# Optimization experiments

Measured on AMD Instinct MI355X. Metric: run time of the kernel, lower is better.

## Reference

```python
import jax, jax.numpy as jnp
import numpy as np


def setup_inputs() -> dict:
    key = jax.random.key(0)
    ks = jax.random.split(key, 7)
    B, d_model, Hs, Ws = 16, 384, 64, 64
    state_dim, d_inner = 64, 768
    L = Hs * Ws
    return {
        "x": jax.random.normal(ks[0], (B, d_model, L), jnp.float32),
        "w_bcdt": jax.random.normal(ks[1], (3 * state_dim, d_model), jnp.float32) * 0.05,
        "w_dw": jax.random.normal(ks[2], (3 * state_dim, 1, 3, 3), jnp.float32) * 0.3,
        "w_hz": jax.random.normal(ks[3], (2 * d_inner, d_model), jnp.float32) * 0.05,
        "w_out": jax.random.normal(ks[4], (d_model, d_inner), jnp.float32) * 0.05,
        "a_param": jax.random.uniform(ks[5], (state_dim,), jnp.float32, 1.0, 16.0),
        "d_param": jnp.ones((1,), jnp.float32),
        "H": Hs,
        "W": Ws,
    }


def reference(x, w_bcdt, w_dw, w_hz, w_out, a_param, d_param, H, W):
    batch, d_model, L = x.shape
    state_dim = a_param.shape[0]
    d_inner = w_out.shape[1]
    conv_dim = 3 * state_dim

    # 1x1 conv projection: (B, 3*state_dim, L)
    bc_dt = jnp.einsum("od,bdl->bol", w_bcdt, x)
    # depthwise 3x3 conv on the (H, W) spatial grid
    bc_dt = bc_dt.reshape(batch, conv_dim, H, W)
    bc_dt = jax.lax.conv_general_dilated(
        bc_dt, w_dw, window_strides=(1, 1), padding=((1, 1), (1, 1)),
        dimension_numbers=("NCHW", "OIHW", "NCHW"),
        feature_group_count=conv_dim,
    ).reshape(batch, conv_dim, L)

    Bm, Cm, dt = jnp.split(bc_dt, 3, axis=1)  # each (B, state_dim, L)
    A = jax.nn.softmax(dt + a_param[None, :, None], axis=-1)
    AB = A * Bm  # (B, state_dim, L)

    # state aggregation: (B, d_model, state_dim)
    h = jnp.einsum("bdl,bsl->bds", x, AB)
    hz = jnp.einsum("od,bds->bos", w_hz, h)  # (B, 2*d_inner, state_dim)
    h_i, z = jnp.split(hz, 2, axis=1)
    h = jnp.einsum("od,bds->bos", w_out, h_i * jax.nn.silu(z) + h_i * d_param)

    # broadcast state back to tokens: (B, d_model, L)
    y = jnp.einsum("bds,bsl->bdl", h, Cm).reshape(batch, d_model, H, W)
    return y, h
```

## Files before the change

kernel.cpp:

```cpp
#include <hip/hip_runtime.h>
#include <hip/hip_bf16.h>

#define BATCH 16
#define DMODEL 384
#define LTOK 4096
#define SDIM 64
#define C3 192
#define DINNER 768

typedef __attribute__((ext_vector_type(8))) short short8;
typedef __attribute__((ext_vector_type(4))) float f32x4;

__device__ __forceinline__ short f2bf(float f) {
    unsigned u = __builtin_bit_cast(unsigned, f);
    u += 0x7fffu + ((u >> 16) & 1u);
    return (short)(u >> 16);
}

template<int BN, int NF, bool AF32, bool BF32, bool ATOMIC>
__global__ __launch_bounds__(256) void gemm_bf16(
    const void* __restrict__ Ap, const void* __restrict__ Bp, float* __restrict__ Cp,
    int M, int N, int K, long sA, long sB, long sC, int nTilesN, int splitK)
{
    const int b = blockIdx.z;
    const int ntile  = blockIdx.x % nTilesN;
    const int kchunk = blockIdx.x / nTilesN;
    const int row0 = blockIdx.y << 6;
    const int col0 = ntile * BN;
    const int kPer = K / splitK;
    const int kBeg = kchunk * kPer, kEnd = kBeg + kPer;

    __shared__ short As[64][40];
    __shared__ short Bs[BN][40];

    const int t = threadIdx.x;
    const int wid = t >> 6, lane = t & 63;
    const int lr = lane & 15;
    const int lk = (lane >> 4) << 3;

    f32x4 acc[4][NF];
#pragma unroll
    for (int i = 0; i < 4; i++)
#pragma unroll
        for (int j = 0; j < NF; j++)
#pragma unroll
            for (int r = 0; r < 4; r++) acc[i][j][r] = 0.f;

    for (int kt = kBeg; kt < kEnd; kt += 32) {
        {
            const int arow = t >> 2, akb = (t & 3) << 3;
            if constexpr (AF32) {
                const float* s = (const float*)Ap + b * sA + (long)(row0 + arow) * K + kt + akb;
                short8 v;
#pragma unroll
                for (int j = 0; j < 8; j++) v[j] = f2bf(s[j]);
                *(short8*)&As[arow][akb] = v;
            } else {
                const short* s = (const short*)Ap + b * sA + (long)(row0 + arow) * K + kt + akb;
                *(short8*)&As[arow][akb] = *(const short8*)s;
            }
        }
#pragma unroll
        for (int rr = 0; rr < BN / 64; rr++) {
            const int u = t + rr * 256;
            const int brow = u >> 2, bkb = (u & 3) << 3;
            if constexpr (BF32) {
                const float* s = (const float*)Bp + b * sB + (long)(col0 + brow) * K + kt + bkb;
                short8 v;
#pragma unroll
                for (int j = 0; j < 8; j++) v[j] = f2bf(s[j]);
                *(short8*)&Bs[brow][bkb] = v;
            } else {
                const short* s = (const short*)Bp + b * sB + (long)(col0 + brow) * K + kt + bkb;
                *(short8*)&Bs[brow][bkb] = *(const short8*)s;
            }
        }
        __syncthreads();

        short8 af[4], bfr[NF];
#pragma unroll
        for (int mi = 0; mi < 4; mi++) af[mi] = *(const short8*)&As[mi * 16 + lr][lk];
#pragma unroll
        for (int ni = 0; ni < NF; ni++) bfr[ni] = *(const short8*)&Bs[wid * (BN / 4) + ni * 16 + lr][lk];
#pragma unroll
        for (int mi = 0; mi < 4; mi++)
#pragma unroll
            for (int ni = 0; ni < NF; ni++)
                acc[mi][ni] = __builtin_amdgcn_mfma_f32_16x16x32_bf16(af[mi], bfr[ni], acc[mi][ni], 0, 0, 0);
        __syncthreads();
    }

    float* Cb = Cp + b * sC;
#pragma unroll
    for (int mi = 0; mi < 4; mi++)
#pragma unroll
        for (int ni = 0; ni < NF; ni++)
#pragma unroll
            for (int r = 0; r < 4; r++) {
                const long row = row0 + mi * 16 + ((lane >> 4) << 2) + r;
                const long col = col0 + wid * (BN / 4) + ni * 16 + lr;
                if constexpr (ATOMIC) atomicAdd(&Cb[row * N + col], acc[mi][ni][r]);
                else                  Cb[row * N + col] = acc[mi][ni][r];
            }
}

__global__ __launch_bounds__(256) void transpose_x(const float* __restrict__ x, short* __restrict__ xbT)
{
    const int b = blockIdx.z;
    const int l0 = blockIdx.x << 6, d0 = blockIdx.y << 6;
    __shared__ float tl[64][65];
    const int t = threadIdx.x, c = t & 63, r0 = t >> 6;
    const float* ip = x + ((long)b * DMODEL + d0) * LTOK + l0;
    for (int d = r0; d < 64; d += 4) tl[d][c] = ip[(long)d * LTOK + c];
    __syncthreads();
    short* op = xbT + ((long)b * LTOK + l0) * DMODEL + d0;
    for (int l = r0; l < 64; l += 4) op[(long)l * DMODEL + c] = f2bf(tl[c][l]);
}

__global__ __launch_bounds__(256) void dwconv3x3(
    const float* __restrict__ in, const float* __restrict__ w, float* __restrict__ out)
{
    const int bc = blockIdx.x;
    const int c = bc % C3;
    __shared__ float tile[64 * 64];
    __shared__ float wc[9];
    const float* ip = in + (long)bc * 4096;
    for (int i = threadIdx.x; i < 4096; i += 256) tile[i] = ip[i];
    if (threadIdx.x < 9) wc[threadIdx.x] = w[c * 9 + threadIdx.x];
    __syncthreads();
    float* op = out + (long)bc * 4096;
    for (int i = threadIdx.x; i < 4096; i += 256) {
        int y = i >> 6, x = i & 63;
        float s = 0.f;
#pragma unroll
        for (int dy = -1; dy <= 1; dy++)
#pragma unroll
            for (int dx = -1; dx <= 1; dx++) {
                int yy = y + dy, xx = x + dx;
                if (yy >= 0 && yy < 64 && xx >= 0 && xx < 64)
                    s += tile[yy * 64 + xx] * wc[(dy + 1) * 3 + (dx + 1)];
            }
        op[i] = s;
    }
}

__global__ __launch_bounds__(256) void softmax_ab(
    const float* __restrict__ conv, short* __restrict__ AB)
{
    const int b = blockIdx.x >> 6, s = blockIdx.x & 63;
    const float* dt = conv + ((long)b * C3 + 128 + s) * (long)LTOK;
    const float* Bm = conv + ((long)b * C3 + s) * (long)LTOK;
    short* ab = AB + ((long)b * SDIM + s) * (long)LTOK;
    const int t = threadIdx.x;

    float v[16];
    float mx = -1e30f;
#pragma unroll
    for (int i = 0; i < 16; i++) { v[i] = dt[t + i * 256]; mx = fmaxf(mx, v[i]); }
#pragma unroll
    for (int o = 32; o > 0; o >>= 1) mx = fmaxf(mx, __shfl_xor(mx, o));
    __shared__ float redm[4];
    const int wid = t >> 6;
    if ((t & 63) == 0) redm[wid] = mx;
    __syncthreads();
    mx = fmaxf(fmaxf(redm[0], redm[1]), fmaxf(redm[2], redm[3]));

    float sum = 0.f;
#pragma unroll
    for (int i = 0; i < 16; i++) { v[i] = __expf(v[i] - mx); sum += v[i]; }
#pragma unroll
    for (int o = 32; o > 0; o >>= 1) sum += __shfl_xor(sum, o);
    __shared__ float reds[4];
    if ((t & 63) == 0) reds[wid] = sum;
    __syncthreads();
    sum = reds[0] + reds[1] + reds[2] + reds[3];
    const float inv = 1.0f / sum;
#pragma unroll
    for (int i = 0; i < 16; i++)
        ab[t + i * 256] = f2bf(v[i] * inv * Bm[t + i * 256]);
}

__global__ __launch_bounds__(256) void gate_k(
    const float* __restrict__ hzT, const float* __restrict__ d_param, float* __restrict__ gT)
{
    const long i = (long)blockIdx.x * 256 + threadIdx.x;
    const long b = i / (SDIM * DINNER), r = i % (SDIM * DINNER);
    const long s = r / DINNER, o = r % DINNER;
    const float* hp = hzT + b * (SDIM * 2L * DINNER) + s * (2L * DINNER);
    const float hi = hp[o];
    const float z  = hp[DINNER + o];
    const float sil = z / (1.f + __expf(-z));
    gT[i] = hi * (sil + d_param[0]);
}

__global__ __launch_bounds__(256) void transpose_hout(
    const float* __restrict__ houtT, float* __restrict__ hout, short* __restrict__ hb)
{
    const int b = blockIdx.y, d0 = blockIdx.x << 6;
    __shared__ float tl[64][65];
    const int t = threadIdx.x, c = t & 63, r0 = t >> 6;
    const float* ip = houtT + (long)b * SDIM * DMODEL + d0;
    for (int s = r0; s < 64; s += 4) tl[s][c] = ip[(long)s * DMODEL + c];
    __syncthreads();
    float* op = hout + ((long)b * DMODEL + d0) * SDIM;
    short* ob = hb + ((long)b * DMODEL + d0) * SDIM;
    for (int d = r0; d < 64; d += 4) {
        float v = tl[c][d];
        op[(long)d * SDIM + c] = v;
        ob[(long)d * SDIM + c] = f2bf(v);
    }
}

__global__ __launch_bounds__(256) void transpose_cm(
    const float* __restrict__ conv, short* __restrict__ CmT)
{
    const int b = blockIdx.y, l0 = blockIdx.x << 6;
    __shared__ float tl[64][65];
    const int t = threadIdx.x, c = t & 63, r0 = t >> 6;
    const float* ip = conv + ((long)b * C3 + SDIM) * LTOK + l0;
    for (int s = r0; s < 64; s += 4) tl[s][c] = ip[(long)s * LTOK + c];
    __syncthreads();
    short* op = CmT + ((long)b * LTOK + l0) * SDIM;
    for (int l = r0; l < 64; l += 4) op[(long)l * SDIM + c] = f2bf(tl[c][l]);
}

extern "C" void kernel_launch(void* const* d_in, const int* in_sizes, int n_in,
                              void* d_out, int out_size, void* d_ws, size_t ws_size,
                              hipStream_t stream) {
    const float* x      = (const float*)d_in[0];
    const float* w_bcdt = (const float*)d_in[1];
    const float* w_dw   = (const float*)d_in[2];
    const float* w_hz   = (const float*)d_in[3];
    const float* w_out  = (const float*)d_in[4];
    const float* dparam = (const float*)d_in[6];

    char* ws = (char*)d_ws;
    short* xbT  = (short*)ws;
    float* conv = (float*)ws;
    float* bcdt  = (float*)(ws + 50331648);
    short* AB    = (short*)(ws + 50331648);
    short* CmT   = (short*)(ws + 58720256);
    float* hT    = (float*)(ws + 67108864);
    float* hzT   = (float*)(ws + 68681728);
    float* gT    = (float*)(ws + 74973184);
    float* houtT = (float*)(ws + 78118912);
    short* hb    = (short*)(ws + 79691776);

    float* y    = (float*)d_out;
    float* hout = (float*)d_out + 25165824;

    transpose_x<<<dim3(64, 6, 16), 256, 0, stream>>>(x, xbT);

    gemm_bf16<128, 2, true, false, false><<<dim3(32, 3, BATCH), 256, 0, stream>>>(
        w_bcdt, xbT, bcdt, C3, LTOK, DMODEL,
        0L, (long)LTOK * DMODEL, (long)C3 * LTOK, 32, 1);

    dwconv3x3<<<dim3(BATCH * C3), 256, 0, stream>>>(bcdt, w_dw, conv);

    softmax_ab<<<dim3(BATCH * SDIM), 256, 0, stream>>>(conv, AB);

    hipMemsetAsync(hT, 0, (size_t)BATCH * SDIM * DMODEL * 4, stream);
    gemm_bf16<128, 2, false, true, true><<<dim3(3 * 8, 1, BATCH), 256, 0, stream>>>(
        AB, x, hT, SDIM, DMODEL, LTOK,
        (long)SDIM * LTOK, (long)DMODEL * LTOK, (long)SDIM * DMODEL, 3, 8);

    gemm_bf16<128, 2, true, true, false><<<dim3(12, 1, BATCH), 256, 0, stream>>>(
        hT, w_hz, hzT, SDIM, 2 * DINNER, DMODEL,
        (long)SDIM * DMODEL, 0L, (long)SDIM * 2 * DINNER, 12, 1);

    gate_k<<<dim3((BATCH * SDIM * DINNER) / 256), 256, 0, stream>>>(hzT, dparam, gT);

    gemm_bf16<128, 2, true, true, false><<<dim3(3, 1, BATCH), 256, 0, stream>>>(
        gT, w_out, houtT, SDIM, DMODEL, DINNER,
        (long)SDIM * DINNER, 0L, (long)SDIM * DMODEL, 3, 1);

    transpose_hout<<<dim3(6, 16), 256, 0, stream>>>(houtT, hout, hb);

    transpose_cm<<<dim3(64, 16), 256, 0, stream>>>(conv, CmT);

    gemm_bf16<128, 2, false, false, false><<<dim3(32, 6, BATCH), 256, 0, stream>>>(
        hb, CmT, y, DMODEL, LTOK, SDIM,
        (long)DMODEL * SDIM, (long)LTOK * SDIM, (long)DMODEL * LTOK, 32, 1);
}
```

Baseline: 356.3 us.

## Store projection in bf16, fuse depthwise conv into softmax, widen GEMM tiles

The projection GEMM now writes its output as bf16 instead of fp32. The depthwise conv for the B and dt channels is fused into the softmax kernel, which reads the bf16 projection into shared memory and computes both convolutions on the fly, so the fp32 conv intermediate is no longer written and read back. A separate kernel convolves only the Cm channels. The first and last GEMMs use 256-wide N tiles with four fragments per wave. This cuts intermediate memory traffic but adds bf16 rounding before the conv and raises per-block register and LDS use.

```diff
diff --git a/kernel.cpp b/kernel.cpp
--- a/kernel.cpp
+++ b/kernel.cpp
@@ -16,10 +16,13 @@
     u += 0x7fffu + ((u >> 16) & 1u);
     return (short)(u >> 16);
 }
-
-template<int BN, int NF, bool AF32, bool BF32, bool ATOMIC>
+__device__ __forceinline__ float bf2f(short s) {
+    return __builtin_bit_cast(float, ((unsigned)(unsigned short)s) << 16);
+}
+
+template<int BN, int NF, bool AF32, bool BF32, int CMODE>
 __global__ __launch_bounds__(256) void gemm_bf16(
-    const void* __restrict__ Ap, const void* __restrict__ Bp, float* __restrict__ Cp,
+    const void* __restrict__ Ap, const void* __restrict__ Bp, void* __restrict__ Cp,
     int M, int N, int K, long sA, long sB, long sC, int nTilesN, int splitK)
 {
     const int b = blockIdx.z;
@@ -90,7 +93,6 @@
         __syncthreads();
     }
 
-    float* Cb = Cp + b * sC;
 #pragma unroll
     for (int mi = 0; mi < 4; mi++)
 #pragma unroll
@@ -99,8 +101,9 @@
             for (int r = 0; r < 4; r++) {
                 const long row = row0 + mi * 16 + ((lane >> 4) << 2) + r;
                 const long col = col0 + wid * (BN / 4) + ni * 16 + lr;
-                if constexpr (ATOMIC) atomicAdd(&Cb[row * N + col], acc[mi][ni][r]);
-                else                  Cb[row * N + col] = acc[mi][ni][r];
+                if constexpr (CMODE == 1)      atomicAdd((float*)Cp + b * sC + row * N + col, acc[mi][ni][r]);
+                else if constexpr (CMODE == 2) *((short*)Cp + b * sC + row * N + col) = f2bf(acc[mi][ni][r]);
+                else                           *((float*)Cp + b * sC + row * N + col) = acc[mi][ni][r];
             }
 }
 
@@ -117,49 +120,47 @@
     for (int l = r0; l < 64; l += 4) op[(long)l * DMODEL + c] = f2bf(tl[c][l]);
 }
 
-__global__ __launch_bounds__(256) void dwconv3x3(
-    const float* __restrict__ in, const float* __restrict__ w, float* __restrict__ out)
-{
-    const int bc = blockIdx.x;
-    const int c = bc % C3;
-    __shared__ float tile[64 * 64];
-    __shared__ float wc[9];
-    const float* ip = in + (long)bc * 4096;
-    for (int i = threadIdx.x; i < 4096; i += 256) tile[i] = ip[i];
-    if (threadIdx.x < 9) wc[threadIdx.x] = w[c * 9 + threadIdx.x];
-    __syncthreads();
-    float* op = out + (long)bc * 4096;
-    for (int i = threadIdx.x; i < 4096; i += 256) {
-        int y = i >> 6, x = i & 63;
-        float s = 0.f;
+__global__ __launch_bounds__(256) void conv_softmax_ab(
+    const short* __restrict__ bcdt, const float* __restrict__ w_dw, short* __restrict__ AB)
+{
+    const int b = blockIdx.x >> 6, s = blockIdx.x & 63;
+    __shared__ float pB[4096];
+    __shared__ float pD[4096];
+    __shared__ float wB[9], wD[9];
+    __shared__ float redm[4], reds[4];
+    const int t = threadIdx.x;
+
+    const short* srcB = bcdt + ((long)b * C3 + s) * 4096;
+    const short* srcD = bcdt + ((long)b * C3 + 128 + s) * 4096;
+#pragma unroll
+    for (int j = 0; j < 2; j++) {
+        const int o = (t + j * 256) * 8;
+        short8 vb = *(const short8*)(srcB + o);
+        short8 vd = *(const short8*)(srcD + o);
+#pragma unroll
+        for (int e = 0; e < 8; e++) { pB[o + e] = bf2f(vb[e]); pD[o + e] = bf2f(vd[e]); }
+    }
+    if (t < 9) { wB[t] = w_dw[s * 9 + t]; wD[t] = w_dw[(128 + s) * 9 + t]; }
+    __syncthreads();
+
+    float v[16];
+    float mx = -1e30f;
+#pragma unroll
+    for (int i = 0; i < 16; i++) {
+        const int l = t + i * 256, y = l >> 6, x = l & 63;
+        float sacc = 0.f;
 #pragma unroll
         for (int dy = -1; dy <= 1; dy++)
 #pragma unroll
             for (int dx = -1; dx <= 1; dx++) {
                 int yy = y + dy, xx = x + dx;
                 if (yy >= 0 && yy < 64 && xx >= 0 && xx < 64)
-                    s += tile[yy * 64 + xx] * wc[(dy + 1) * 3 + (dx + 1)];
-            }
-        op[i] = s;
-    }
-}
-
-__global__ __launch_bounds__(256) void softmax_ab(
-    const float* __restrict__ conv, short* __restrict__ AB)
-{
-    const int b = blockIdx.x >> 6, s = blockIdx.x & 63;
-    const float* dt = conv + ((long)b * C3 + 128 + s) * (long)LTOK;
-    const float* Bm = conv + ((long)b * C3 + s) * (long)LTOK;
-    short* ab = AB + ((long)b * SDIM + s) * (long)LTOK;
-    const int t = threadIdx.x;
-
-    float v[16];
-    float mx = -1e30f;
-#pragma unroll
-    for (int i = 0; i < 16; i++) { v[i] = dt[t + i * 256]; mx = fmaxf(mx, v[i]); }
+                    sacc += pD[yy * 64 + xx] * wD[(dy + 1) * 3 + (dx + 1)];
+            }
+        v[i] = sacc; mx = fmaxf(mx, sacc);
+    }
 #pragma unroll
     for (int o = 32; o > 0; o >>= 1) mx = fmaxf(mx, __shfl_xor(mx, o));
-    __shared__ float redm[4];
     const int wid = t >> 6;
     if ((t & 63) == 0) redm[wid] = mx;
     __syncthreads();
@@ -170,14 +171,73 @@
     for (int i = 0; i < 16; i++) { v[i] = __expf(v[i] - mx); sum += v[i]; }
 #pragma unroll
     for (int o = 32; o > 0; o >>= 1) sum += __shfl_xor(sum, o);
-    __shared__ float reds[4];
     if ((t & 63) == 0) reds[wid] = sum;
     __syncthreads();
     sum = reds[0] + reds[1] + reds[2] + reds[3];
     const float inv = 1.0f / sum;
-#pragma unroll
-    for (int i = 0; i < 16; i++)
-        ab[t + i * 256] = f2bf(v[i] * inv * Bm[t + i * 256]);
+
+    short* ab = AB + ((long)b * SDIM + s) * (long)LTOK;
+#pragma unroll
+    for (int i = 0; i < 16; i++) {
+        const int l = t + i * 256, y = l >> 6, x = l & 63;
+        float uacc = 0.f;
+#pragma unroll
+        for (int dy = -1; dy <= 1; dy++)
+#pragma unroll
+            for (int dx = -1; dx <= 1; dx++) {
+                int yy = y + dy, xx = x + dx;
+                if (yy >= 0 && yy < 64 && xx >= 0 && xx < 64)
+                    uacc += pB[yy * 64 + xx] * wB[(dy + 1) * 3 + (dx + 1)];
+            }
+        ab[l] = f2bf(v[i] * inv * uacc);
+    }
+}
+
+__global__ __launch_bounds__(256) void dwconv_cm(
+    const short* __restrict__ bcdt, const float* __restrict__ w, float* __restrict__ convCm)
+{
+    const int bc = blockIdx.x;
+    const int b = bc >> 6, cc = bc & 63;
+    __shared__ float tile[4096];
+    __shared__ float wc[9];
+    const short* ip = bcdt + ((long)b * C3 + 64 + cc) * 4096;
+    const int t = threadIdx.x;
+#pragma unroll
+    for (int j = 0; j < 2; j++) {
+        const int o = (t + j * 256) * 8;
+        short8 vv = *(const short8*)(ip + o);
+#pragma unroll
+        for (int e = 0; e < 8; e++) tile[o + e] = bf2f(vv[e]);
+    }
+    if (t < 9) wc[t] = w[(64 + cc) * 9 + t];
+    __syncthreads();
+    float* op = convCm + (long)bc * 4096;
+    for (int i = t; i < 4096; i += 256) {
+        int y = i >> 6, x = i & 63;
+        float sacc = 0.f;
+#pragma unroll
+        for (int dy = -1; dy <= 1; dy++)
+#pragma unroll
+            for (int dx = -1; dx <= 1; dx++) {
+                int yy = y + dy, xx = x + dx;
+                if (yy >= 0 && yy < 64 && xx >= 0 && xx < 64)
+                    sacc += tile[yy * 64 + xx] * wc[(dy + 1) * 3 + (dx + 1)];
+            }
+        op[i] = sacc;
+    }
+}
+
+__global__ __launch_bounds__(256) void transpose_cm(
+    const float* __restrict__ convCm, short* __restrict__ CmT)
+{
+    const int b = blockIdx.y, l0 = blockIdx.x << 6;
+    __shared__ float tl[64][65];
+    const int t = threadIdx.x, c = t & 63, r0 = t >> 6;
+    const float* ip = convCm + (long)b * SDIM * LTOK + l0;
+    for (int s = r0; s < 64; s += 4) tl[s][c] = ip[(long)s * LTOK + c];
+    __syncthreads();
+    short* op = CmT + ((long)b * LTOK + l0) * SDIM;
+    for (int l = r0; l < 64; l += 4) op[(long)l * SDIM + c] = f2bf(tl[c][l]);
 }
 
 __global__ __launch_bounds__(256) void gate_k(
@@ -209,19 +269,6 @@
         op[(long)d * SDIM + c] = v;
         ob[(long)d * SDIM + c] = f2bf(v);
     }
-}
-
-__global__ __launch_bounds__(256) void transpose_cm(
-    const float* __restrict__ conv, short* __restrict__ CmT)
-{
-    const int b = blockIdx.y, l0 = blockIdx.x << 6;
-    __shared__ float tl[64][65];
-    const int t = threadIdx.x, c = t & 63, r0 = t >> 6;
-    const float* ip = conv + ((long)b * C3 + SDIM) * LTOK + l0;
-    for (int s = r0; s < 64; s += 4) tl[s][c] = ip[(long)s * LTOK + c];
-    __syncthreads();
-    short* op = CmT + ((long)b * LTOK + l0) * SDIM;
-    for (int l = r0; l < 64; l += 4) op[(long)l * SDIM + c] = f2bf(tl[c][l]);
 }
 
 extern "C" void kernel_launch(void* const* d_in, const int* in_sizes, int n_in,
@@ -235,50 +282,50 @@
     const float* dparam = (const float*)d_in[6];
 
     char* ws = (char*)d_ws;
-    short* xbT  = (short*)ws;
-    float* conv = (float*)ws;
-    float* bcdt  = (float*)(ws + 50331648);
-    short* AB    = (short*)(ws + 50331648);
-    short* CmT   = (short*)(ws + 58720256);
-    float* hT    = (float*)(ws + 67108864);
-    float* hzT   = (float*)(ws + 68681728);
-    float* gT    = (float*)(ws + 74973184);
-    float* houtT = (float*)(ws + 78118912);
-    short* hb    = (short*)(ws + 79691776);
+    short* xbT    = (short*)(ws);
+    short* bcdt   = (short*)(ws + 50331648);
+    short* AB     = (short*)(ws + 75497472);
+    float* convCm = (float*)(ws + 83886080);
+    short* CmT    = (short*)(ws + 100663296);
+    float* hT     = (float*)(ws + 109051904);
+    float* hzT    = (float*)(ws + 110624768);
+    float* gT     = (float*)(ws + 116916224);
+    float* houtT  = (float*)(ws + 120061952);
+    short* hb     = (short*)(ws + 121634816);
 
     float* y    = (float*)d_out;
     float* hout = (float*)d_out + 25165824;
 
     transpose_x<<<dim3(64, 6, 16), 256, 0, stream>>>(x, xbT);
 
-    gemm_bf16<128, 2, true, false, false><<<dim3(32, 3, BATCH), 256, 0, stream>>>(
+    gemm_bf16<256, 4, true, false, 2><<<dim3(16, 3, BATCH), 256, 0, stream>>>(
         w_bcdt, xbT, bcdt, C3, LTOK, DMODEL,
-        0L, (long)LTOK * DMODEL, (long)C3 * LTOK, 32, 1);
-
-    dwconv3x3<<<dim3(BATCH * C3), 256, 0, stream>>>(bcdt, w_dw, conv);
-
-    softmax_ab<<<dim3(BATCH * SDIM), 256, 0, stream>>>(conv, AB);
+        0L, (long)LTOK * DMODEL, (long)C3 * LTOK, 16, 1);
+
+    conv_softmax_ab<<<dim3(BATCH * SDIM), 256, 0, stream>>>(bcdt, w_dw, AB);
+
+    dwconv_cm<<<dim3(BATCH * SDIM), 256, 0, stream>>>(bcdt, w_dw, convCm);
+
+    transpose_cm<<<dim3(64, 16), 256, 0, stream>>>(convCm, CmT);
 
     hipMemsetAsync(hT, 0, (size_t)BATCH * SDIM * DMODEL * 4, stream);
-    gemm_bf16<128, 2, false, true, true><<<dim3(3 * 8, 1, BATCH), 256, 0, stream>>>(
+    gemm_bf16<128, 2, false, true, 1><<<dim3(3 * 8, 1, BATCH), 256, 0, stream>>>(
         AB, x, hT, SDIM, DMODEL, LTOK,
         (long)SDIM * LTOK, (long)DMODEL * LTOK, (long)SDIM * DMODEL, 3, 8);
 
-    gemm_bf16<128, 2, true, true, false><<<dim3(12, 1, BATCH), 256, 0, stream>>>(
+    gemm_bf16<128, 2, true, true, 0><<<dim3(12, 1, BATCH), 256, 0, stream>>>(
         hT, w_hz, hzT, SDIM, 2 * DINNER, DMODEL,
         (long)SDIM * DMODEL, 0L, (long)SDIM * 2 * DINNER, 12, 1);
 
     gate_k<<<dim3((BATCH * SDIM * DINNER) / 256), 256, 0, stream>>>(hzT, dparam, gT);
 
-    gemm_bf16<128, 2, true, true, false><<<dim3(3, 1, BATCH), 256, 0, stream>>>(
+    gemm_bf16<128, 2, true, true, 0><<<dim3(3, 1, BATCH), 256, 0, stream>>>(
         gT, w_out, houtT, SDIM, DMODEL, DINNER,
         (long)SDIM * DINNER, 0L, (long)SDIM * DMODEL, 3, 1);
 
     transpose_hout<<<dim3(6, 16), 256, 0, stream>>>(houtT, hout, hb);
 
-    transpose_cm<<<dim3(64, 16), 256, 0, stream>>>(conv, CmT);
-
-    gemm_bf16<128, 2, false, false, false><<<dim3(32, 6, BATCH), 256, 0, stream>>>(
+    gemm_bf16<256, 4, false, false, 0><<<dim3(16, 6, BATCH), 256, 0, stream>>>(
         hb, CmT, y, DMODEL, LTOK, SDIM,
-        (long)DMODEL * SDIM, (long)LTOK * SDIM, (long)DMODEL * LTOK, 32, 1);
-}
+        (long)DMODEL * SDIM, (long)LTOK * SDIM, (long)DMODEL * LTOK, 16, 1);
+}
```

Measured after the change: 353.0 us. Within noise of the previous version (-0.9%).
